# Optimization experiments

Hardware: AMD Instinct MI355X
Metric: run time of the kernel (lower is better)

## Reference

```python
import jax, jax.numpy as jnp
import numpy as np

B, S, H = 2, 2048, 2048
E, K = 16, 4
I_MOE, I_SH = 1408, 5632


def setup_inputs() -> dict:
    key = jax.random.key(0)
    ks = jax.random.split(key, 9)
    def w(k, shape, fan_in):
        return jax.random.normal(k, shape, jnp.float32) * (fan_in ** -0.5)
    return {
        "hidden_states": jax.random.normal(ks[0], (B, S, H), jnp.float32),
        "router_w": w(ks[1], (E, H), H),           # router gate weight [E, H]
        "w_gate": w(ks[2], (E, H, I_MOE), H),       # stacked expert gate_proj
        "w_up": w(ks[3], (E, H, I_MOE), H),         # stacked expert up_proj
        "w_down": w(ks[4], (E, I_MOE, H), I_MOE),   # stacked expert down_proj
        "sh_gate": w(ks[5], (H, I_SH), H),          # shared expert gate_proj
        "sh_up": w(ks[6], (H, I_SH), H),            # shared expert up_proj
        "sh_down": w(ks[7], (I_SH, H), I_SH),       # shared expert down_proj
        "sh_gate_w": w(ks[8], (H, 1), H),           # shared_expert_gate (Linear H->1)
    }


def reference(hidden_states, router_w, w_gate, w_up, w_down,
              sh_gate, sh_up, sh_down, sh_gate_w):
    orig = hidden_states.shape
    h = hidden_states.reshape(-1, orig[-1])  # [N, H]
    N = h.shape[0]

    # --- router: softmax (fp32) -> top-k -> renormalise ---
    logits = h @ router_w.T                               # [N, E]
    probs = jax.nn.softmax(logits.astype(jnp.float32), axis=-1)
    top_vals, top_idx = jax.lax.top_k(probs, K)           # [N, K]
    top_vals = top_vals / jnp.maximum(top_vals.sum(-1, keepdims=True), 1e-9)
    top_vals = top_vals.astype(h.dtype)

    # combine weights: [N, E], gate value where routed, 0 elsewhere
    comb = jnp.zeros((N, E), h.dtype).at[jnp.arange(N)[:, None], top_idx].add(top_vals)

    # --- routed experts (dense-over-experts, masked combine == gather/scatter math) ---
    g = jnp.einsum('nh,ehi->eni', h, w_gate)              # [E, N, I]
    u = jnp.einsum('nh,ehi->eni', h, w_up)                # [E, N, I]
    y = jnp.einsum('eni,eih->enh', jax.nn.silu(g) * u, w_down)  # [E, N, H]
    routed = jnp.einsum('enh,ne->nh', y, comb)            # [N, H]

    # --- shared expert with sigmoid gate ---
    shared = (jax.nn.silu(h @ sh_gate) * (h @ sh_up)) @ sh_down  # [N, H]
    sg = jax.nn.sigmoid(h @ sh_gate_w)                    # [N, 1]

    return (routed + sg * shared).reshape(orig)
```

## Files before the change

### kernel.cpp

```cpp
#include <hip/hip_runtime.h>
#include <stdint.h>


#define N_TOK 4096
#define H_DIM 2048
#define E_NUM 16
#define TOPK  4
#define IMOE  1408
#define ISH   5632
#define SLOTS (N_TOK*TOPK)

#define MT 128
#define BK 64

typedef __attribute__((ext_vector_type(8))) short bf16x8;
typedef __attribute__((ext_vector_type(4))) float f32x4;

static __device__ inline unsigned short f2bf(float f) {
    union { float f; unsigned u; } v; v.f = f;
    unsigned r = v.u + 0x7fffu + ((v.u >> 16) & 1u);
    return (unsigned short)(r >> 16);
}

static __device__ inline void glds16(const unsigned short* g, unsigned short* l) {
    __builtin_amdgcn_global_load_lds(
        (const __attribute__((address_space(1))) void*)g,
        (__attribute__((address_space(3))) void*)l, 16, 0, 0);
}

static __device__ inline bool decode_tile(int bx, int by, int NX, int NYact,
                                          int& nt, int& mt) {
    int f = by * NX + bx;
    int NB = NX * NYact;
    if (f >= NB) return false;
    int q = NB >> 3, rr = NB & 7;
    int x = f & 7, s = f >> 3;
    int L = (x < rr ? x * (q + 1) : rr * (q + 1) + (x - rr) * q) + s;
    const int GM = 8;
    int G = GM * NX;
    int g = L / G, r2 = L - g * G;
    int gm = NYact - g * GM; if (gm > GM) gm = GM;
    nt = r2 / gm;
    mt = g * GM + (r2 - nt * gm);
    return true;
}

__global__ void cvt_h_kernel(const float* __restrict__ in, unsigned short* __restrict__ out, int n4) {
    int i = blockIdx.x * blockDim.x + threadIdx.x;
    if (i < n4) {
        float4 v = *(const float4*)(in + (size_t)i * 4);
        ushort4 o; o.x = f2bf(v.x); o.y = f2bf(v.y); o.z = f2bf(v.z); o.w = f2bf(v.w);
        *(ushort4*)(out + (size_t)i * 4) = o;
    }
}

__global__ void transpose_cvt_kernel(const float* __restrict__ in, unsigned short* __restrict__ out,
                                     int R, int C) {
    __shared__ float tile[32][33];
    const float* ip = in + (size_t)blockIdx.z * R * C;
    unsigned short* op = out + (size_t)blockIdx.z * R * C;
    int cb = blockIdx.x * 32, rb = blockIdx.y * 32;
    int tx = threadIdx.x, ty = threadIdx.y;
    for (int i = 0; i < 4; i++)
        tile[ty + i * 8][tx] = ip[(size_t)(rb + ty + i * 8) * C + cb + tx];
    __syncthreads();
    for (int i = 0; i < 4; i++)
        op[(size_t)(cb + ty + i * 8) * R + rb + tx] = f2bf(tile[tx][ty + i * 8]);
}

__global__ __launch_bounds__(256) void router_kernel(
    const float* __restrict__ h, const float* __restrict__ rw, const float* __restrict__ gw,
    int* __restrict__ topk_idx, float* __restrict__ topk_w,
    float* __restrict__ sg, int* __restrict__ counts) {
    int t = threadIdx.x;
    int wv = t >> 6, lane = t & 63;
    int tokw = lane >> 4, part = lane & 15;
    int n = blockIdx.x * 16 + wv * 4 + tokw;
    const float* hp = h + (size_t)n * H_DIM;

    float acc[17];
#pragma unroll
    for (int e = 0; e < 17; e++) acc[e] = 0.f;

    for (int i = 0; i < 32; i++) {
        int j = i * 64 + part * 4;
        float4 hv = *(const float4*)(hp + j);
#pragma unroll
        for (int e = 0; e < E_NUM; e++) {
            float4 w4 = *(const float4*)(rw + (size_t)e * H_DIM + j);
            acc[e] += hv.x * w4.x + hv.y * w4.y + hv.z * w4.z + hv.w * w4.w;
        }
        float4 g4 = *(const float4*)(gw + j);
        acc[16] += hv.x * g4.x + hv.y * g4.y + hv.z * g4.z + hv.w * g4.w;
    }
#pragma unroll
    for (int d = 8; d; d >>= 1)
#pragma unroll
        for (int e = 0; e < 17; e++)
            acc[e] += __shfl_down(acc[e], d, 16);

    if (part == 0) {
        float m = acc[0];
#pragma unroll
        for (int i = 1; i < E_NUM; i++) m = fmaxf(m, acc[i]);
        float p[E_NUM]; float s = 0.f;
#pragma unroll
        for (int i = 0; i < E_NUM; i++) { p[i] = expf(acc[i] - m); s += p[i]; }
        float invs = 1.f / s;
#pragma unroll
        for (int i = 0; i < E_NUM; i++) p[i] *= invs;
        int idx[TOPK]; float val[TOPK]; float vs = 0.f; unsigned used = 0;
#pragma unroll
        for (int k = 0; k < TOPK; k++) {
            int bi = 0; float bv = -1.f;
#pragma unroll
            for (int i = 0; i < E_NUM; i++)
                if (!((used >> i) & 1u) && p[i] > bv) { bv = p[i]; bi = i; }
            idx[k] = bi; val[k] = bv; vs += bv; used |= (1u << bi);
        }
        float inv = 1.f / fmaxf(vs, 1e-9f);
#pragma unroll
        for (int k = 0; k < TOPK; k++) {
            topk_idx[n * TOPK + k] = idx[k];
            topk_w[n * TOPK + k] = val[k] * inv;
            atomicAdd(&counts[idx[k]], 1);
        }
        sg[n] = 1.f / (1.f + expf(-acc[16]));
    }
}

__global__ void scan_kernel(const int* __restrict__ counts, int* __restrict__ offsets,
                            int* __restrict__ cursor) {
    int s = 0;
    for (int e = 0; e < E_NUM; e++) { offsets[e] = s; cursor[e] = s; s += counts[e]; }
}

__global__ void bucketize_kernel(const int* __restrict__ topk_idx, const float* __restrict__ topk_w,
                                 int* __restrict__ cursor, int* __restrict__ slot_tok,
                                 float* __restrict__ slot_w) {
    int n = blockIdx.x * blockDim.x + threadIdx.x;
    if (n >= N_TOK) return;
    for (int k = 0; k < TOPK; k++) {
        int e = topk_idx[n * TOPK + k];
        int s = atomicAdd(&cursor[e], 1);
        slot_tok[s] = n;
        slot_w[s] = topk_w[n * TOPK + k];
    }
}

__global__ __launch_bounds__(256) void gather_kernel(const unsigned short* __restrict__ hbf,
                                                     const int* __restrict__ slot_tok,
                                                     unsigned short* __restrict__ A) {
    int s = blockIdx.x;
    int tok = slot_tok[s];
    const uint4* src = (const uint4*)(hbf + (size_t)tok * H_DIM);
    uint4* dst = (uint4*)(A + (size_t)s * H_DIM);
    dst[threadIdx.x] = src[threadIdx.x];
}

__global__ __launch_bounds__(256, 2) void gemm_dual_kernel(
    const unsigned short* __restrict__ A, const unsigned short* __restrict__ Bg,
    const unsigned short* __restrict__ Bu, unsigned short* __restrict__ act,
    const int* __restrict__ counts, const int* __restrict__ offsets,
    int K, int N, int fixedM) {
    int e = blockIdx.z;
    int c, off;
    if (counts) { c = counts[e]; off = offsets[e]; } else { c = fixedM; off = 0; }
    int NYact = (c + MT - 1) / MT;
    int nt, mt;
    if (!decode_tile(blockIdx.x, blockIdx.y, gridDim.x, NYact, nt, mt)) return;

    const unsigned short* Ab = A + (size_t)off * K;
    const unsigned short* Bgb = Bg + (size_t)e * (size_t)N * K;
    const unsigned short* Bub = Bu + (size_t)e * (size_t)N * K;
    unsigned short* actb = act + (size_t)off * N;

    __shared__ __align__(16) unsigned short As[MT * BK];
    __shared__ __align__(16) unsigned short Bgs[64 * BK];
    __shared__ __align__(16) unsigned short Bus[64 * BK];

    int t = threadIdx.x;
    int wave = t >> 6, lane = t & 63;
    int wm = wave >> 1, wn = wave & 1;
    int quad = lane >> 4, l16 = lane & 15;

    f32x4 accg[4][2], accu[4][2];
    for (int i = 0; i < 4; i++) for (int j = 0; j < 2; j++) { accg[i][j] = (f32x4)0.f; accu[i][j] = (f32x4)0.f; }

    int m0 = mt * MT, n0 = nt * 64;
    int rA[4], cA[4];
    for (int j = 0; j < 4; j++) { int s = t + 256 * j; rA[j] = s >> 3; cA[j] = (s & 7) ^ (rA[j] & 7); }
    int rB[2], cB[2];
    for (int j = 0; j < 2; j++) { int s = t + 256 * j; rB[j] = s >> 3; cB[j] = (s & 7) ^ (rB[j] & 7); }

    for (int kt = 0; kt < K; kt += BK) {
        __syncthreads();
        for (int j = 0; j < 4; j++)
            glds16(&Ab[(size_t)(m0 + rA[j]) * K + kt + cA[j] * 8], &As[(t + 256 * j) * 8]);
        for (int j = 0; j < 2; j++) {
            glds16(&Bgb[(size_t)(n0 + rB[j]) * K + kt + cB[j] * 8], &Bgs[(t + 256 * j) * 8]);
            glds16(&Bub[(size_t)(n0 + rB[j]) * K + kt + cB[j] * 8], &Bus[(t + 256 * j) * 8]);
        }
        __syncthreads();
#pragma unroll
        for (int ks = 0; ks < 2; ks++) {
            int lbase = (ks << 2) | quad;
            bf16x8 af[4], bgf[2], buf[2];
            for (int mi = 0; mi < 4; mi++) {
                int rowl = wm * 64 + mi * 16 + l16;
                af[mi] = *(const bf16x8*)&As[rowl * BK + ((lbase ^ (rowl & 7)) * 8)];
            }
            for (int ni = 0; ni < 2; ni++) {
                int rowl = wn * 32 + ni * 16 + l16;
                int co = (lbase ^ (rowl & 7)) * 8;
                bgf[ni] = *(const bf16x8*)&Bgs[rowl * BK + co];
                buf[ni] = *(const bf16x8*)&Bus[rowl * BK + co];
            }
            for (int mi = 0; mi < 4; mi++)
                for (int ni = 0; ni < 2; ni++) {
                    accg[mi][ni] = __builtin_amdgcn_mfma_f32_16x16x32_bf16(af[mi], bgf[ni], accg[mi][ni], 0, 0, 0);
                    accu[mi][ni] = __builtin_amdgcn_mfma_f32_16x16x32_bf16(af[mi], buf[ni], accu[mi][ni], 0, 0, 0);
                }
        }
    }
    for (int mi = 0; mi < 4; mi++) {
        for (int r = 0; r < 4; r++) {
            int rl = m0 + wm * 64 + mi * 16 + quad * 4 + r;
            if (rl < c) {
                size_t rowbase = (size_t)rl * N + n0 + wn * 32 + l16;
                for (int ni = 0; ni < 2; ni++) {
                    float g = accg[mi][ni][r];
                    float u = accu[mi][ni][r];
                    float a = (g / (1.f + __expf(-g))) * u;
                    actb[rowbase + ni * 16] = f2bf(a);
                }
            }
        }
    }
}

__global__ __launch_bounds__(256, 2) void gemm_down_kernel(
    const unsigned short* __restrict__ Aact, const unsigned short* __restrict__ Bd,
    float* __restrict__ out,
    const int* __restrict__ counts, const int* __restrict__ offsets,
    const int* __restrict__ slot_tok, const float* __restrict__ slot_w,
    const float* __restrict__ sg,
    int K, int N, int fixedM) {
    int e = blockIdx.z;
    bool routed = (counts != nullptr);
    int c, off;
    if (routed) { c = counts[e]; off = offsets[e]; } else { c = fixedM; off = 0; }
    int NYact = (c + MT - 1) / MT;
    int nt, mt;
    if (!decode_tile(blockIdx.x, blockIdx.y, gridDim.x, NYact, nt, mt)) return;

    const unsigned short* Ab = Aact + (size_t)off * K;
    const unsigned short* Bb = Bd + (size_t)e * (size_t)N * K;

    __shared__ __align__(16) unsigned short As[MT * BK];
    __shared__ __align__(16) unsigned short Bs[MT * BK];

    int t = threadIdx.x;
    int wave = t >> 6, lane = t & 63;
    int wm = wave >> 1, wn = wave & 1;
    int quad = lane >> 4, l16 = lane & 15;

    f32x4 acc[4][4];
    for (int i = 0; i < 4; i++) for (int j = 0; j < 4; j++) acc[i][j] = (f32x4)0.f;

    int m0 = mt * MT, n0 = nt * MT;
    int rA[4], cA[4];
    for (int j = 0; j < 4; j++) { int s = t + 256 * j; rA[j] = s >> 3; cA[j] = (s & 7) ^ (rA[j] & 7); }

    for (int kt = 0; kt < K; kt += BK) {
        __syncthreads();
        for (int j = 0; j < 4; j++) {
            glds16(&Ab[(size_t)(m0 + rA[j]) * K + kt + cA[j] * 8], &As[(t + 256 * j) * 8]);
            glds16(&Bb[(size_t)(n0 + rA[j]) * K + kt + cA[j] * 8], &Bs[(t + 256 * j) * 8]);
        }
        __syncthreads();
#pragma unroll
        for (int ks = 0; ks < 2; ks++) {
            int lbase = (ks << 2) | quad;
            bf16x8 af[4], bf[4];
            for (int mi = 0; mi < 4; mi++) {
                int rowl = wm * 64 + mi * 16 + l16;
                af[mi] = *(const bf16x8*)&As[rowl * BK + ((lbase ^ (rowl & 7)) * 8)];
            }
            for (int ni = 0; ni < 4; ni++) {
                int rowl = wn * 64 + ni * 16 + l16;
                bf[ni] = *(const bf16x8*)&Bs[rowl * BK + ((lbase ^ (rowl & 7)) * 8)];
            }
            for (int mi = 0; mi < 4; mi++)
                for (int ni = 0; ni < 4; ni++)
                    acc[mi][ni] = __builtin_amdgcn_mfma_f32_16x16x32_bf16(af[mi], bf[ni], acc[mi][ni], 0, 0, 0);
        }
    }
    for (int mi = 0; mi < 4; mi++) {
        for (int r = 0; r < 4; r++) {
            int rl = m0 + wm * 64 + mi * 16 + quad * 4 + r;
            if (rl < c) {
                int col = n0 + wn * 64 + l16;
                if (routed) {
                    int s = off + rl;
                    int tok = slot_tok[s];
                    float w = slot_w[s];
                    float* ob = out + (size_t)tok * N + col;
                    for (int ni = 0; ni < 4; ni++)
                        atomicAdd(ob + ni * 16, w * acc[mi][ni][r]);
                } else {
                    float w = sg[rl];
                    float* ob = out + (size_t)rl * N + col;
                    for (int ni = 0; ni < 4; ni++)
                        ob[ni * 16] += w * acc[mi][ni][r];
                }
            }
        }
    }
}

extern "C" void kernel_launch(void* const* d_in, const int* in_sizes, int n_in,
                              void* d_out, int out_size, void* d_ws, size_t ws_size,
                              hipStream_t stream) {
    const float* h   = (const float*)d_in[0];
    const float* rw  = (const float*)d_in[1];
    const float* wg  = (const float*)d_in[2];
    const float* wu  = (const float*)d_in[3];
    const float* wd  = (const float*)d_in[4];
    const float* shg = (const float*)d_in[5];
    const float* shu = (const float*)d_in[6];
    const float* shd = (const float*)d_in[7];
    const float* sgw = (const float*)d_in[8];
    float* out = (float*)d_out;

    char* ws = (char*)d_ws;
    size_t off = 0;
    auto alloc = [&](size_t b) { size_t o = off; off += (b + 255) & ~(size_t)255; return (void*)(ws + o); };

    int*   counts   = (int*)  alloc(E_NUM * 4);
    int*   offsets  = (int*)  alloc(E_NUM * 4);
    int*   cursor   = (int*)  alloc(E_NUM * 4);
    int*   topk_idx = (int*)  alloc((size_t)N_TOK * TOPK * 4);
    float* topk_w   = (float*)alloc((size_t)N_TOK * TOPK * 4);
    float* sg       = (float*)alloc((size_t)N_TOK * 4);
    int*   slot_tok = (int*)  alloc((size_t)SLOTS * 4);
    float* slot_w   = (float*)alloc((size_t)SLOTS * 4);
    unsigned short* h_bf  = (unsigned short*)alloc((size_t)N_TOK * H_DIM * 2);
    unsigned short* wgT   = (unsigned short*)alloc((size_t)E_NUM * IMOE * H_DIM * 2);
    unsigned short* wuT   = (unsigned short*)alloc((size_t)E_NUM * IMOE * H_DIM * 2);
    unsigned short* wdT   = (unsigned short*)alloc((size_t)E_NUM * H_DIM * IMOE * 2);
    unsigned short* shGT  = (unsigned short*)alloc((size_t)ISH * H_DIM * 2);
    unsigned short* shUT  = (unsigned short*)alloc((size_t)ISH * H_DIM * 2);
    unsigned short* shDT  = (unsigned short*)alloc((size_t)H_DIM * ISH * 2);
    unsigned short* Agath = (unsigned short*)alloc((size_t)(SLOTS + MT) * H_DIM * 2);
    unsigned short* actR  = (unsigned short*)alloc((size_t)(SLOTS + MT) * IMOE * 2);
    unsigned short* actS  = (unsigned short*)alloc((size_t)N_TOK * ISH * 2);
    (void)ws_size; (void)in_sizes; (void)n_in; (void)out_size;

    hipMemsetAsync(out, 0, (size_t)N_TOK * H_DIM * 4, stream);
    hipMemsetAsync(counts, 0, E_NUM * 4, stream);

    cvt_h_kernel<<<(N_TOK * H_DIM / 4 + 255) / 256, 256, 0, stream>>>(h, h_bf, N_TOK * H_DIM / 4);
    transpose_cvt_kernel<<<dim3(IMOE / 32, H_DIM / 32, E_NUM), dim3(32, 8), 0, stream>>>(wg, wgT, H_DIM, IMOE);
    transpose_cvt_kernel<<<dim3(IMOE / 32, H_DIM / 32, E_NUM), dim3(32, 8), 0, stream>>>(wu, wuT, H_DIM, IMOE);
    transpose_cvt_kernel<<<dim3(H_DIM / 32, IMOE / 32, E_NUM), dim3(32, 8), 0, stream>>>(wd, wdT, IMOE, H_DIM);
    transpose_cvt_kernel<<<dim3(ISH / 32, H_DIM / 32, 1), dim3(32, 8), 0, stream>>>(shg, shGT, H_DIM, ISH);
    transpose_cvt_kernel<<<dim3(ISH / 32, H_DIM / 32, 1), dim3(32, 8), 0, stream>>>(shu, shUT, H_DIM, ISH);
    transpose_cvt_kernel<<<dim3(H_DIM / 32, ISH / 32, 1), dim3(32, 8), 0, stream>>>(shd, shDT, ISH, H_DIM);

    router_kernel<<<N_TOK / 16, 256, 0, stream>>>(h, rw, sgw, topk_idx, topk_w, sg, counts);
    scan_kernel<<<1, 1, 0, stream>>>(counts, offsets, cursor);
    bucketize_kernel<<<N_TOK / 256, 256, 0, stream>>>(topk_idx, topk_w, cursor, slot_tok, slot_w);
    gather_kernel<<<SLOTS, 256, 0, stream>>>(h_bf, slot_tok, Agath);

    gemm_dual_kernel<<<dim3(IMOE / 64, N_TOK / MT, E_NUM), 256, 0, stream>>>(
        Agath, wgT, wuT, actR, counts, offsets, H_DIM, IMOE, 0);
    gemm_dual_kernel<<<dim3(ISH / 64, N_TOK / MT, 1), 256, 0, stream>>>(
        h_bf, shGT, shUT, actS, nullptr, nullptr, H_DIM, ISH, N_TOK);
    gemm_down_kernel<<<dim3(H_DIM / MT, N_TOK / MT, E_NUM), 256, 0, stream>>>(
        actR, wdT, out, counts, offsets, slot_tok, slot_w, nullptr, IMOE, H_DIM, 0);
    gemm_down_kernel<<<dim3(H_DIM / MT, N_TOK / MT, 1), 256, 0, stream>>>(
        actS, shDT, out, nullptr, nullptr, nullptr, nullptr, sg, ISH, H_DIM, N_TOK);
}
```

Measured before the change: 1.495 ms.

## Replace atomic scatter with per-slot outputs and combine kernel; vectorize weight transpose

The routed down-projection now writes each slot's result into a dense fp32 buffer instead of atomically adding into the output. The shared down-projection writes into a separate buffer that reuses the routed activation storage. A new combine kernel then gathers each token's four expert rows, applies the routing and sigmoid gate weights, and writes the output directly, so the output memset is no longer needed. Separately, the weight transpose/convert kernel moves to 64x64 tiles with float4 loads and ushort4 stores to cut memory transactions. The cost is extra global traffic for the intermediate slot buffer, one more launch, and possible LDS bank conflicts in the new transpose layout.

Result: faster. 1.459 ms (-2.4%).

```diff
diff --git a/kernel.cpp b/kernel.cpp
--- a/kernel.cpp
+++ b/kernel.cpp
@@ -54,18 +54,34 @@
     }
 }
 
-__global__ void transpose_cvt_kernel(const float* __restrict__ in, unsigned short* __restrict__ out,
-                                     int R, int C) {
-    __shared__ float tile[32][33];
+__global__ __launch_bounds__(256) void transpose_cvt_kernel(
+    const float* __restrict__ in, unsigned short* __restrict__ out, int R, int C) {
+    __shared__ float tile[64][65];
     const float* ip = in + (size_t)blockIdx.z * R * C;
     unsigned short* op = out + (size_t)blockIdx.z * R * C;
-    int cb = blockIdx.x * 32, rb = blockIdx.y * 32;
-    int tx = threadIdx.x, ty = threadIdx.y;
-    for (int i = 0; i < 4; i++)
-        tile[ty + i * 8][tx] = ip[(size_t)(rb + ty + i * 8) * C + cb + tx];
+    int cb = blockIdx.x * 64, rb = blockIdx.y * 64;
+    int tid = threadIdx.x;
+    int lr = tid >> 4, lc = tid & 15;
+#pragma unroll
+    for (int p = 0; p < 4; p++) {
+        int r = p * 16 + lr;
+        float4 v = *(const float4*)(ip + (size_t)(rb + r) * C + cb + lc * 4);
+        tile[r][lc * 4 + 0] = v.x;
+        tile[r][lc * 4 + 1] = v.y;
+        tile[r][lc * 4 + 2] = v.z;
+        tile[r][lc * 4 + 3] = v.w;
+    }
     __syncthreads();
-    for (int i = 0; i < 4; i++)
-        op[(size_t)(cb + ty + i * 8) * R + rb + tx] = f2bf(tile[tx][ty + i * 8]);
+#pragma unroll
+    for (int p = 0; p < 4; p++) {
+        int oc = p * 16 + lr;
+        ushort4 o;
+        o.x = f2bf(tile[lc * 4 + 0][oc]);
+        o.y = f2bf(tile[lc * 4 + 1][oc]);
+        o.z = f2bf(tile[lc * 4 + 2][oc]);
+        o.w = f2bf(tile[lc * 4 + 3][oc]);
+        *(ushort4*)(op + (size_t)(cb + oc) * R + rb + lc * 4) = o;
+    }
 }
 
 __global__ __launch_bounds__(256) void router_kernel(
@@ -135,16 +151,16 @@
     for (int e = 0; e < E_NUM; e++) { offsets[e] = s; cursor[e] = s; s += counts[e]; }
 }
 
-__global__ void bucketize_kernel(const int* __restrict__ topk_idx, const float* __restrict__ topk_w,
+__global__ void bucketize_kernel(const int* __restrict__ topk_idx,
                                  int* __restrict__ cursor, int* __restrict__ slot_tok,
-                                 float* __restrict__ slot_w) {
+                                 int* __restrict__ tok_slot) {
     int n = blockIdx.x * blockDim.x + threadIdx.x;
     if (n >= N_TOK) return;
     for (int k = 0; k < TOPK; k++) {
         int e = topk_idx[n * TOPK + k];
         int s = atomicAdd(&cursor[e], 1);
         slot_tok[s] = n;
-        slot_w[s] = topk_w[n * TOPK + k];
+        tok_slot[n * TOPK + k] = s;
     }
 }
 
@@ -241,15 +257,12 @@
 
 __global__ __launch_bounds__(256, 2) void gemm_down_kernel(
     const unsigned short* __restrict__ Aact, const unsigned short* __restrict__ Bd,
-    float* __restrict__ out,
+    float* __restrict__ Y,
     const int* __restrict__ counts, const int* __restrict__ offsets,
-    const int* __restrict__ slot_tok, const float* __restrict__ slot_w,
-    const float* __restrict__ sg,
     int K, int N, int fixedM) {
     int e = blockIdx.z;
-    bool routed = (counts != nullptr);
     int c, off;
-    if (routed) { c = counts[e]; off = offsets[e]; } else { c = fixedM; off = 0; }
+    if (counts) { c = counts[e]; off = offsets[e]; } else { c = fixedM; off = 0; }
     int NYact = (c + MT - 1) / MT;
     int nt, mt;
     if (!decode_tile(blockIdx.x, blockIdx.y, gridDim.x, NYact, nt, mt)) return;
@@ -301,21 +314,40 @@
             int rl = m0 + wm * 64 + mi * 16 + quad * 4 + r;
             if (rl < c) {
                 int col = n0 + wn * 64 + l16;
-                if (routed) {
-                    int s = off + rl;
-                    int tok = slot_tok[s];
-                    float w = slot_w[s];
-                    float* ob = out + (size_t)tok * N + col;
-                    for (int ni = 0; ni < 4; ni++)
-                        atomicAdd(ob + ni * 16, w * acc[mi][ni][r]);
-                } else {
-                    float w = sg[rl];
-                    float* ob = out + (size_t)rl * N + col;
-                    for (int ni = 0; ni < 4; ni++)
-                        ob[ni * 16] += w * acc[mi][ni][r];
-                }
-            }
-        }
+                float* ob = Y + (size_t)(off + rl) * N + col;
+                for (int ni = 0; ni < 4; ni++)
+                    ob[ni * 16] = acc[mi][ni][r];
+            }
+        }
+    }
+}
+
+__global__ __launch_bounds__(256) void combine_kernel(
+    const float* __restrict__ ySlot, const float* __restrict__ ySh,
+    const int* __restrict__ tok_slot, const float* __restrict__ topk_w,
+    const float* __restrict__ sgv, float* __restrict__ out) {
+    int n = blockIdx.x;
+    int s0 = tok_slot[n * TOPK + 0], s1 = tok_slot[n * TOPK + 1];
+    int s2 = tok_slot[n * TOPK + 2], s3 = tok_slot[n * TOPK + 3];
+    float w0 = topk_w[n * TOPK + 0], w1 = topk_w[n * TOPK + 1];
+    float w2 = topk_w[n * TOPK + 2], w3 = topk_w[n * TOPK + 3];
+    float g = sgv[n];
+    const float4* p0 = (const float4*)(ySlot + (size_t)s0 * H_DIM);
+    const float4* p1 = (const float4*)(ySlot + (size_t)s1 * H_DIM);
+    const float4* p2 = (const float4*)(ySlot + (size_t)s2 * H_DIM);
+    const float4* p3 = (const float4*)(ySlot + (size_t)s3 * H_DIM);
+    const float4* ps = (const float4*)(ySh + (size_t)n * H_DIM);
+    float4* po = (float4*)(out + (size_t)n * H_DIM);
+#pragma unroll
+    for (int it = 0; it < H_DIM / 4 / 256; it++) {
+        int i = it * 256 + threadIdx.x;
+        float4 a = p0[i], b = p1[i], cc = p2[i], d = p3[i], s = ps[i];
+        float4 r;
+        r.x = w0 * a.x + w1 * b.x + w2 * cc.x + w3 * d.x + g * s.x;
+        r.y = w0 * a.y + w1 * b.y + w2 * cc.y + w3 * d.y + g * s.y;
+        r.z = w0 * a.z + w1 * b.z + w2 * cc.z + w3 * d.z + g * s.z;
+        r.w = w0 * a.w + w1 * b.w + w2 * cc.w + w3 * d.w + g * s.w;
+        po[i] = r;
     }
 }
 
@@ -344,7 +376,7 @@
     float* topk_w   = (float*)alloc((size_t)N_TOK * TOPK * 4);
     float* sg       = (float*)alloc((size_t)N_TOK * 4);
     int*   slot_tok = (int*)  alloc((size_t)SLOTS * 4);
-    float* slot_w   = (float*)alloc((size_t)SLOTS * 4);
+    int*   tok_slot = (int*)  alloc((size_t)SLOTS * 4);
     unsigned short* h_bf  = (unsigned short*)alloc((size_t)N_TOK * H_DIM * 2);
     unsigned short* wgT   = (unsigned short*)alloc((size_t)E_NUM * IMOE * H_DIM * 2);
     unsigned short* wuT   = (unsigned short*)alloc((size_t)E_NUM * IMOE * H_DIM * 2);
@@ -355,22 +387,23 @@
     unsigned short* Agath = (unsigned short*)alloc((size_t)(SLOTS + MT) * H_DIM * 2);
     unsigned short* actR  = (unsigned short*)alloc((size_t)(SLOTS + MT) * IMOE * 2);
     unsigned short* actS  = (unsigned short*)alloc((size_t)N_TOK * ISH * 2);
+    float* ySlot = (float*)alloc((size_t)SLOTS * H_DIM * 4);
+    float* ySh   = (float*)actR;
     (void)ws_size; (void)in_sizes; (void)n_in; (void)out_size;
 
-    hipMemsetAsync(out, 0, (size_t)N_TOK * H_DIM * 4, stream);
     hipMemsetAsync(counts, 0, E_NUM * 4, stream);
 
     cvt_h_kernel<<<(N_TOK * H_DIM / 4 + 255) / 256, 256, 0, stream>>>(h, h_bf, N_TOK * H_DIM / 4);
-    transpose_cvt_kernel<<<dim3(IMOE / 32, H_DIM / 32, E_NUM), dim3(32, 8), 0, stream>>>(wg, wgT, H_DIM, IMOE);
-    transpose_cvt_kernel<<<dim3(IMOE / 32, H_DIM / 32, E_NUM), dim3(32, 8), 0, stream>>>(wu, wuT, H_DIM, IMOE);
-    transpose_cvt_kernel<<<dim3(H_DIM / 32, IMOE / 32, E_NUM), dim3(32, 8), 0, stream>>>(wd, wdT, IMOE, H_DIM);
-    transpose_cvt_kernel<<<dim3(ISH / 32, H_DIM / 32, 1), dim3(32, 8), 0, stream>>>(shg, shGT, H_DIM, ISH);
-    transpose_cvt_kernel<<<dim3(ISH / 32, H_DIM / 32, 1), dim3(32, 8), 0, stream>>>(shu, shUT, H_DIM, ISH);
-    transpose_cvt_kernel<<<dim3(H_DIM / 32, ISH / 32, 1), dim3(32, 8), 0, stream>>>(shd, shDT, ISH, H_DIM);
+    transpose_cvt_kernel<<<dim3(IMOE / 64, H_DIM / 64, E_NUM), 256, 0, stream>>>(wg, wgT, H_DIM, IMOE);
+    transpose_cvt_kernel<<<dim3(IMOE / 64, H_DIM / 64, E_NUM), 256, 0, stream>>>(wu, wuT, H_DIM, IMOE);
+    transpose_cvt_kernel<<<dim3(H_DIM / 64, IMOE / 64, E_NUM), 256, 0, stream>>>(wd, wdT, IMOE, H_DIM);
+    transpose_cvt_kernel<<<dim3(ISH / 64, H_DIM / 64, 1), 256, 0, stream>>>(shg, shGT, H_DIM, ISH);
+    transpose_cvt_kernel<<<dim3(ISH / 64, H_DIM / 64, 1), 256, 0, stream>>>(shu, shUT, H_DIM, ISH);
+    transpose_cvt_kernel<<<dim3(H_DIM / 64, ISH / 64, 1), 256, 0, stream>>>(shd, shDT, ISH, H_DIM);
 
     router_kernel<<<N_TOK / 16, 256, 0, stream>>>(h, rw, sgw, topk_idx, topk_w, sg, counts);
     scan_kernel<<<1, 1, 0, stream>>>(counts, offsets, cursor);
-    bucketize_kernel<<<N_TOK / 256, 256, 0, stream>>>(topk_idx, topk_w, cursor, slot_tok, slot_w);
+    bucketize_kernel<<<N_TOK / 256, 256, 0, stream>>>(topk_idx, cursor, slot_tok, tok_slot);
     gather_kernel<<<SLOTS, 256, 0, stream>>>(h_bf, slot_tok, Agath);
 
     gemm_dual_kernel<<<dim3(IMOE / 64, N_TOK / MT, E_NUM), 256, 0, stream>>>(
@@ -378,7 +411,8 @@
     gemm_dual_kernel<<<dim3(ISH / 64, N_TOK / MT, 1), 256, 0, stream>>>(
         h_bf, shGT, shUT, actS, nullptr, nullptr, H_DIM, ISH, N_TOK);
     gemm_down_kernel<<<dim3(H_DIM / MT, N_TOK / MT, E_NUM), 256, 0, stream>>>(
-        actR, wdT, out, counts, offsets, slot_tok, slot_w, nullptr, IMOE, H_DIM, 0);
+        actR, wdT, ySlot, counts, offsets, IMOE, H_DIM, 0);
     gemm_down_kernel<<<dim3(H_DIM / MT, N_TOK / MT, 1), 256, 0, stream>>>(
-        actS, shDT, out, nullptr, nullptr, nullptr, nullptr, sg, ISH, H_DIM, N_TOK);
-}
+        actS, shDT, ySh, nullptr, nullptr, ISH, H_DIM, N_TOK);
+    combine_kernel<<<N_TOK, 256, 0, stream>>>(ySlot, ySh, tok_slot, topk_w, sg, out);
+}
```
